# Kernel tuning notes

Measured on AMD Instinct MI355X. Metric: run time of the kernel, lower is better.

Reference implementation:

```python
import jax, jax.numpy as jnp
from jax import lax
import numpy as np

B, S, V, H, C = 128, 512, 128, 1024, 10
E = H // 4  # embed_dim = hidden_dim / 4 per the module


def setup_inputs() -> dict:
    key = jax.random.key(0)
    ks = jax.random.split(key, 16)

    def kaiming(k, shape):
        fan_in = shape[0]
        return jax.random.normal(k, shape, dtype=jnp.float32) * np.sqrt(2.0 / fan_in)

    return {
        "x": jax.random.randint(ks[0], (B, 1, S), 0, V),
        "embedding": jax.random.normal(ks[1], (V, E), dtype=jnp.float32),
        "W_gx": kaiming(ks[2], (E, H)), "W_gh": kaiming(ks[3], (H, H)), "b_g": jnp.zeros((H,), jnp.float32),
        "W_ix": kaiming(ks[4], (E, H)), "W_ih": kaiming(ks[5], (H, H)), "b_i": jnp.zeros((H,), jnp.float32),
        "W_fx": kaiming(ks[6], (E, H)), "W_fh": kaiming(ks[7], (H, H)), "b_f": jnp.zeros((H,), jnp.float32),
        "W_ox": kaiming(ks[8], (E, H)), "W_oh": kaiming(ks[9], (H, H)), "b_o": jnp.zeros((H,), jnp.float32),
        "W_ph": kaiming(ks[10], (H, C)), "b_p": jnp.zeros((C,), jnp.float32),
    }


def reference(x, embedding, W_gx, W_gh, b_g, W_ix, W_ih, b_i,
              W_fx, W_fh, b_f, W_ox, W_oh, b_o, W_ph, b_p):
    batch = x.shape[0]
    hid = W_gh.shape[0]
    # embed whole sequence at once: [B, S, E]
    xe = embedding[x[:, 0, :]]
    # fuse the 4 input-side GEMMs into one: [B, S, 4H] (precomputable, parallel over time)
    Wx = jnp.concatenate([W_gx, W_ix, W_fx, W_ox], axis=1)  # [E, 4H]
    Wh = jnp.concatenate([W_gh, W_ih, W_fh, W_oh], axis=1)  # [H, 4H]
    b = jnp.concatenate([b_g, b_i, b_f, b_o])               # [4H]
    xproj = jnp.einsum('bse,ef->sbf', xe, Wx) + b           # [S, B, 4H] (time-major for scan)

    def step(carry, xp_t):
        h, c = carry
        z = xp_t + h @ Wh  # [B, 4H]
        g = jnp.tanh(z[:, :hid])
        i = jax.nn.sigmoid(z[:, hid:2 * hid])
        f = jax.nn.sigmoid(z[:, 2 * hid:3 * hid])
        o = jax.nn.sigmoid(z[:, 3 * hid:])
        c = g * i + c * f
        h = jnp.tanh(c) * o
        return (h, c), None

    h0 = jnp.zeros((batch, hid), xproj.dtype)
    c0 = jnp.zeros((batch, hid), xproj.dtype)
    (h, _), _ = lax.scan(step, (h0, c0), xproj)

    p = h @ W_ph + b_p
    return jax.nn.log_softmax(p, axis=1)
```

## Files before the change

kernel.cpp:

```cpp
#include <hip/hip_runtime.h>

#define H_ 1024
#define B_ 128
#define S_ 512
#define V_ 128
#define E_ 256

#define ZSH_OFF 0
#define TSH_OFF 67584
#define HSH_OFF 135168
#define XSH_OFF 136192
#define SMEM_TOTAL 136256

#define HXBUF 131072

typedef __bf16 bf16x8 __attribute__((ext_vector_type(8)));
typedef float f32x4 __attribute__((ext_vector_type(4)));
typedef unsigned long long ull;

__device__ __forceinline__ uint4 cload16(const unsigned short* p) {
  uint4 r;
  asm volatile("global_load_dwordx4 %0, %1, off sc0 sc1"
               : "=v"(r) : "v"(p) : "memory");
  return r;
}
__device__ __forceinline__ void cstore8(unsigned short* p, ull v) {
  __hip_atomic_store((ull*)p, v, __ATOMIC_RELAXED, __HIP_MEMORY_SCOPE_AGENT);
}

__device__ __forceinline__ unsigned short f2bf(float f) {
  unsigned u = __float_as_uint(f);
  u += 0x7fffu + ((u >> 16) & 1u);
  return (unsigned short)(u >> 16);
}
__device__ __forceinline__ float sigf(float x) { return 1.0f / (1.0f + __expf(-x)); }
__device__ __forceinline__ float tanhfast(float x) { return 1.0f - 2.0f / (1.0f + __expf(2.0f * x)); }

__global__ void __launch_bounds__(256)
prep_kernel(const float* __restrict__ emb,
            const float* __restrict__ Wgx, const float* __restrict__ Wix,
            const float* __restrict__ Wfx, const float* __restrict__ Wox,
            const float* __restrict__ bg, const float* __restrict__ bi,
            const float* __restrict__ bf_, const float* __restrict__ bo,
            const float* __restrict__ Wgh, const float* __restrict__ Wih,
            const float* __restrict__ Wfh, const float* __restrict__ Woh,
            const int* __restrict__ x,
            float* __restrict__ tokproj, unsigned short* __restrict__ WhT,
            int* __restrict__ xT) {
  __shared__ float esh[E_];
  const int bid = blockIdx.x;
  if (bid < 2048) {
    const int v = bid >> 4;
    const int c = (bid & 15) * 256 + threadIdx.x;
    const int gate = c >> 10;
    const int j = c & 1023;
    const float* W = (gate == 0) ? Wgx : (gate == 1) ? Wix : (gate == 2) ? Wfx : Wox;
    const float* bias = (gate == 0) ? bg : (gate == 1) ? bi : (gate == 2) ? bf_ : bo;
    esh[threadIdx.x] = emb[v * E_ + threadIdx.x];
    __syncthreads();
    float acc = bias[j];
#pragma unroll 4
    for (int e = 0; e < E_; ++e) acc += esh[e] * W[e * H_ + j];
    tokproj[v * 4096 + c] = acc;
  } else if (bid < 6144) {
    const int c = bid - 2048;
    const int gate = c >> 10;
    const int j = c & 1023;
    const float* W = (gate == 0) ? Wgh : (gate == 1) ? Wih : (gate == 2) ? Wfh : Woh;
    for (int k = threadIdx.x; k < H_; k += 256)
      WhT[c * H_ + k] = f2bf(W[k * H_ + j]);
  } else {
    const int id = (bid - 6144) * 256 + threadIdx.x;
    const int s = id >> 7, b = id & 127;
    xT[s * 128 + b] = x[b * S_ + s];
  }
}

__global__ void __launch_bounds__(512, 1)
lstm_scan(const int* __restrict__ xT, const float* __restrict__ tokproj,
          const unsigned short* __restrict__ WhT,
          unsigned short* __restrict__ hX, float* __restrict__ hfin,
          unsigned* __restrict__ pub) {
  extern __shared__ char smem[];
  float* Zsh = (float*)(smem + ZSH_OFF);
  float* tsh = (float*)(smem + TSH_OFF);
  unsigned short* hsh = (unsigned short*)(smem + HSH_OFF);
  int* xsh = (int*)(smem + XSH_OFF);

  const int bid = blockIdx.x;
  const int rg = bid >> 5;
  const int cg = bid & 31;
  const int tid = threadIdx.x;
  const int w = tid >> 6;
  const int lane = tid & 63;
  const int l15 = lane & 15;
  const int lq = lane >> 4;

  for (int it = tid; it < 16384; it += 512) {
    const int v = it >> 7, j = it & 127;
    const int gate = j >> 5, hu = j & 31;
    tsh[(v * 33 + hu) * 4 + gate] = tokproj[v * 4096 + gate * 1024 + cg * 32 + hu];
  }
  uint4 breg[32];
#pragma unroll
  for (int kc = 0; kc < 4; ++kc) {
#pragma unroll
    for (int t = 0; t < 8; ++t) {
      const int j = t * 16 + l15;
      const int c = ((j >> 5) << 10) + cg * 32 + (j & 31);
      breg[kc * 8 + t] =
          *(const uint4*)(WhT + c * 1024 + (w * 4 + kc) * 32 + lq * 8);
    }
  }

  const int row_own = tid >> 5;
  const int hu = tid & 31;
  const int brow = rg * 16 + row_own;
  const int colg = cg * 32 + hu;

  const unsigned* myflag = pub + (rg * 32 + w * 4 + (lane & 3)) * 32;
  const unsigned short* abase[4];
#pragma unroll
  for (int kc = 0; kc < 4; ++kc)
    abase[kc] = hX + (rg * 32 + w * 4 + kc) * 512 + lane * 8;

  float creg = 0.f;
  if (tid < 128) cstore8(hX + bid * 512 + tid * 4, 0ull);
  asm volatile("s_waitcnt vmcnt(0)" ::: "memory");
  __syncthreads();
  if (tid == 0)
    __hip_atomic_store(pub + bid * 32, 1u, __ATOMIC_RELAXED, __HIP_MEMORY_SCOPE_AGENT);

  for (int s = 0; s < S_; ++s) {
    int xv = 0;
    if (tid < 16) xv = xT[s * 128 + rg * 16 + tid];

    const unsigned tgt = (unsigned)(s + 1);
    while (__hip_atomic_load(myflag, __ATOMIC_RELAXED, __HIP_MEMORY_SCOPE_AGENT) < tgt)
      __builtin_amdgcn_s_sleep(1);

    const int soff = (s & 1) * HXBUF;
    uint4 a[4];
#pragma unroll
    for (int kc = 0; kc < 4; ++kc) a[kc] = cload16(abase[kc] + soff);
    asm volatile("s_waitcnt vmcnt(0)" ::: "memory");
    __builtin_amdgcn_sched_barrier(0);
#pragma unroll
    for (int kc = 0; kc < 4; ++kc) {
      asm volatile("" : "+v"(a[kc].x), "+v"(a[kc].y), "+v"(a[kc].z), "+v"(a[kc].w));
    }

    if (tid < 16) xsh[tid] = xv;

    f32x4 acc[8];
#pragma unroll
    for (int t = 0; t < 8; ++t) acc[t] = (f32x4){0.f, 0.f, 0.f, 0.f};
#pragma unroll
    for (int kc = 0; kc < 4; ++kc) {
      const bf16x8 av = __builtin_bit_cast(bf16x8, a[kc]);
#pragma unroll
      for (int t = 0; t < 8; ++t)
        acc[t] = __builtin_amdgcn_mfma_f32_16x16x32_bf16(
            av, __builtin_bit_cast(bf16x8, breg[kc * 8 + t]), acc[t], 0, 0, 0);
    }
#pragma unroll
    for (int r_ = 0; r_ < 4; ++r_) {
      const int row = w * 16 + lq * 4 + r_;
      f32x4 lo = {acc[0][r_], acc[2][r_], acc[4][r_], acc[6][r_]};
      f32x4 hi = {acc[1][r_], acc[3][r_], acc[5][r_], acc[7][r_]};
      *(f32x4*)(Zsh + (row * 33 + l15) * 4) = lo;
      *(f32x4*)(Zsh + (row * 33 + l15 + 16) * 4) = hi;
    }
    __syncthreads();

    {
      const int xb = xsh[row_own];
      f32x4 z4 = *(const f32x4*)(tsh + (xb * 33 + hu) * 4);
#pragma unroll
      for (int w8 = 0; w8 < 8; ++w8)
        z4 += *(const f32x4*)(Zsh + ((w8 * 16 + row_own) * 33 + hu) * 4);
      const float gv = tanhfast(z4[0]);
      const float iv = sigf(z4[1]);
      const float fv = sigf(z4[2]);
      const float ov = sigf(z4[3]);
      creg = gv * iv + creg * fv;
      const float hv = tanhfast(creg) * ov;
      hsh[row_own * 32 + hu] = f2bf(hv);
      if (s == S_ - 1) hfin[brow * H_ + colg] = hv;
    }
    __syncthreads();

    if (tid < 64) {
      const ull* hp = (const ull*)hsh;
      const int si = (tid & 15) * 8 + (tid >> 4) * 2;
      unsigned short* dst = hX + ((s + 1) & 1) * HXBUF + bid * 512 + tid * 8;
      cstore8(dst, hp[si]);
      cstore8(dst + 4, hp[si + 1]);
      asm volatile("s_waitcnt vmcnt(0)" ::: "memory");
      if (tid == 0)
        __hip_atomic_store(pub + bid * 32, (unsigned)(s + 2),
                           __ATOMIC_RELAXED, __HIP_MEMORY_SCOPE_AGENT);
    }
  }
}

__global__ void __launch_bounds__(256)
classify_kernel(const float* __restrict__ hfin, const float* __restrict__ Wph,
                const float* __restrict__ bp, float* __restrict__ out) {
  __shared__ float red[256 * 10];
  const int b = blockIdx.x, tid = threadIdx.x;
  float acc[10];
#pragma unroll
  for (int c = 0; c < 10; ++c) acc[c] = 0.f;
  for (int k = tid; k < H_; k += 256) {
    const float hv = hfin[b * H_ + k];
    const float* w = Wph + k * 10;
#pragma unroll
    for (int c = 0; c < 10; ++c) acc[c] += hv * w[c];
  }
#pragma unroll
  for (int c = 0; c < 10; ++c) red[tid * 10 + c] = acc[c];
  __syncthreads();
  for (int off = 128; off >= 1; off >>= 1) {
    if (tid < off) {
#pragma unroll
      for (int c = 0; c < 10; ++c) red[tid * 10 + c] += red[(tid + off) * 10 + c];
    }
    __syncthreads();
  }
  if (tid == 0) {
    float p[10];
    float m = -1e30f;
#pragma unroll
    for (int c = 0; c < 10; ++c) { p[c] = red[c] + bp[c]; m = fmaxf(m, p[c]); }
    float ssum = 0.f;
#pragma unroll
    for (int c = 0; c < 10; ++c) ssum += __expf(p[c] - m);
    const float lse = m + __logf(ssum);
#pragma unroll
    for (int c = 0; c < 10; ++c) out[b * 10 + c] = p[c] - lse;
  }
}

extern "C" void kernel_launch(void* const* d_in, const int* in_sizes, int n_in,
                              void* d_out, int out_size, void* d_ws, size_t ws_size,
                              hipStream_t stream) {
  (void)in_sizes; (void)n_in; (void)out_size; (void)ws_size;
  const int* x = (const int*)d_in[0];
  const float* emb = (const float*)d_in[1];
  const float* Wgx = (const float*)d_in[2];
  const float* Wgh = (const float*)d_in[3];
  const float* bg = (const float*)d_in[4];
  const float* Wix = (const float*)d_in[5];
  const float* Wih = (const float*)d_in[6];
  const float* bi = (const float*)d_in[7];
  const float* Wfx = (const float*)d_in[8];
  const float* Wfh = (const float*)d_in[9];
  const float* bf_ = (const float*)d_in[10];
  const float* Wox = (const float*)d_in[11];
  const float* Woh = (const float*)d_in[12];
  const float* bo = (const float*)d_in[13];
  const float* Wph = (const float*)d_in[14];
  const float* bp = (const float*)d_in[15];
  float* out = (float*)d_out;

  char* ws = (char*)d_ws;
  float* tokproj = (float*)ws;
  unsigned short* WhT = (unsigned short*)(ws + 2097152);
  unsigned short* hX = (unsigned short*)(ws + 10485760);
  float* hfin = (float*)(ws + 11010048);
  int* xT = (int*)(ws + 11538432);
  unsigned* pub = (unsigned*)(ws + 11800576);

  (void)hipMemsetAsync(pub, 0, 32768, stream);
  (void)hipFuncSetAttribute(reinterpret_cast<const void*>(lstm_scan),
                            hipFuncAttributeMaxDynamicSharedMemorySize, SMEM_TOTAL);

  prep_kernel<<<dim3(6400), dim3(256), 0, stream>>>(
      emb, Wgx, Wix, Wfx, Wox, bg, bi, bf_, bo,
      Wgh, Wih, Wfh, Woh, x, tokproj, WhT, xT);
  lstm_scan<<<dim3(256), dim3(512), SMEM_TOTAL, stream>>>(
      xT, tokproj, WhT, hX, hfin, pub);
  classify_kernel<<<dim3(128), dim3(256), 0, stream>>>(hfin, Wph, bp, out);
}
```

Baseline: 1.709 ms.

## Replace flag-based inter-block sync with NaN-sentinel triple-buffered hidden state

Drops the per-block publish flags and signals readiness through sentinel values in the hidden-state buffers. It uses a triple buffer: each step resets the buffer two steps ahead to 0xFFFF patterns, and consumers spin-reload their h tiles until no sentinel remains. This removes the flag store/load round trip and the wait for the data stores before publishing, which shortens the serial per-step critical path. In exchange, spinning now re-reads full data tiles. Correctness depends on bf16 h never encoding as 0xFFFF and on ordering between the reset and the data stores. A guard counter also breaks out after a bounded number of spins, which could silently consume stale data.

```diff
diff --git a/kernel.cpp b/kernel.cpp
--- a/kernel.cpp
+++ b/kernel.cpp
@@ -17,6 +17,9 @@
 typedef __bf16 bf16x8 __attribute__((ext_vector_type(8)));
 typedef float f32x4 __attribute__((ext_vector_type(4)));
 typedef unsigned long long ull;
+
+#define NANP 0xFFFFFFFFu
+#define NAN8 0xFFFFFFFFFFFFFFFFull
 
 __device__ __forceinline__ uint4 cload16(const unsigned short* p) {
   uint4 r;
@@ -79,8 +82,7 @@
 __global__ void __launch_bounds__(512, 1)
 lstm_scan(const int* __restrict__ xT, const float* __restrict__ tokproj,
           const unsigned short* __restrict__ WhT,
-          unsigned short* __restrict__ hX, float* __restrict__ hfin,
-          unsigned* __restrict__ pub) {
+          unsigned short* __restrict__ hX, float* __restrict__ hfin) {
   extern __shared__ char smem[];
   float* Zsh = (float*)(smem + ZSH_OFF);
   float* tsh = (float*)(smem + TSH_OFF);
@@ -118,32 +120,46 @@
   const int brow = rg * 16 + row_own;
   const int colg = cg * 32 + hu;
 
-  const unsigned* myflag = pub + (rg * 32 + w * 4 + (lane & 3)) * 32;
   const unsigned short* abase[4];
 #pragma unroll
   for (int kc = 0; kc < 4; ++kc)
     abase[kc] = hX + (rg * 32 + w * 4 + kc) * 512 + lane * 8;
 
   float creg = 0.f;
-  if (tid < 128) cstore8(hX + bid * 512 + tid * 4, 0ull);
-  asm volatile("s_waitcnt vmcnt(0)" ::: "memory");
-  __syncthreads();
-  if (tid == 0)
-    __hip_atomic_store(pub + bid * 32, 1u, __ATOMIC_RELAXED, __HIP_MEMORY_SCOPE_AGENT);
+  if (tid < 64) {
+    unsigned short* dst = hX + bid * 512 + tid * 8;
+    cstore8(dst, 0ull);
+    cstore8(dst + 4, 0ull);
+  }
+
+  int bcur = 0;
+  int bnxt = 1;
+  int brst = 2;
 
   for (int s = 0; s < S_; ++s) {
     int xv = 0;
     if (tid < 16) xv = xT[s * 128 + rg * 16 + tid];
 
-    const unsigned tgt = (unsigned)(s + 1);
-    while (__hip_atomic_load(myflag, __ATOMIC_RELAXED, __HIP_MEMORY_SCOPE_AGENT) < tgt)
-      __builtin_amdgcn_s_sleep(1);
-
-    const int soff = (s & 1) * HXBUF;
+    const int soff = bcur * HXBUF;
     uint4 a[4];
-#pragma unroll
-    for (int kc = 0; kc < 4; ++kc) a[kc] = cload16(abase[kc] + soff);
-    asm volatile("s_waitcnt vmcnt(0)" ::: "memory");
+    {
+      int need0 = 1, need1 = 1, need2 = 1, need3 = 1;
+      int guard = 0;
+      for (;;) {
+        if (need0) a[0] = cload16(abase[0] + soff);
+        if (need1) a[1] = cload16(abase[1] + soff);
+        if (need2) a[2] = cload16(abase[2] + soff);
+        if (need3) a[3] = cload16(abase[3] + soff);
+        asm volatile("s_waitcnt vmcnt(0)" ::: "memory");
+        if (need0) need0 = !__all((int)((a[0].x != NANP) & (a[0].z != NANP)));
+        if (need1) need1 = !__all((int)((a[1].x != NANP) & (a[1].z != NANP)));
+        if (need2) need2 = !__all((int)((a[2].x != NANP) & (a[2].z != NANP)));
+        if (need3) need3 = !__all((int)((a[3].x != NANP) & (a[3].z != NANP)));
+        if (!(need0 | need1 | need2 | need3)) break;
+        if (++guard > (1 << 14)) break;
+        __builtin_amdgcn_s_sleep(1);
+      }
+    }
     __builtin_amdgcn_sched_barrier(0);
 #pragma unroll
     for (int kc = 0; kc < 4; ++kc) {
@@ -191,16 +207,17 @@
     __syncthreads();
 
     if (tid < 64) {
+      unsigned short* rdst = hX + brst * HXBUF + bid * 512 + tid * 8;
+      cstore8(rdst, NAN8);
+      cstore8(rdst + 4, NAN8);
+      asm volatile("s_waitcnt vmcnt(0)" ::: "memory");
       const ull* hp = (const ull*)hsh;
       const int si = (tid & 15) * 8 + (tid >> 4) * 2;
-      unsigned short* dst = hX + ((s + 1) & 1) * HXBUF + bid * 512 + tid * 8;
+      unsigned short* dst = hX + bnxt * HXBUF + bid * 512 + tid * 8;
       cstore8(dst, hp[si]);
       cstore8(dst + 4, hp[si + 1]);
-      asm volatile("s_waitcnt vmcnt(0)" ::: "memory");
-      if (tid == 0)
-        __hip_atomic_store(pub + bid * 32, (unsigned)(s + 2),
-                           __ATOMIC_RELAXED, __HIP_MEMORY_SCOPE_AGENT);
-    }
+    }
+    const int t_ = bcur; bcur = bnxt; bnxt = brst; brst = t_;
   }
 }
 
@@ -268,11 +285,10 @@
   float* tokproj = (float*)ws;
   unsigned short* WhT = (unsigned short*)(ws + 2097152);
   unsigned short* hX = (unsigned short*)(ws + 10485760);
-  float* hfin = (float*)(ws + 11010048);
-  int* xT = (int*)(ws + 11538432);
-  unsigned* pub = (unsigned*)(ws + 11800576);
-
-  (void)hipMemsetAsync(pub, 0, 32768, stream);
+  float* hfin = (float*)(ws + 11272192);
+  int* xT = (int*)(ws + 11796480);
+
+  (void)hipMemsetAsync(hX, 0xFF, 786432, stream);
   (void)hipFuncSetAttribute(reinterpret_cast<const void*>(lstm_scan),
                             hipFuncAttributeMaxDynamicSharedMemorySize, SMEM_TOTAL);
 
@@ -280,6 +296,6 @@
       emb, Wgx, Wix, Wfx, Wox, bg, bi, bf_, bo,
       Wgh, Wih, Wfh, Woh, x, tokproj, WhT, xT);
   lstm_scan<<<dim3(256), dim3(512), SMEM_TOTAL, stream>>>(
-      xT, tokproj, WhT, hX, hfin, pub);
+      xT, tokproj, WhT, hX, hfin);
   classify_kernel<<<dim3(128), dim3(256), 0, stream>>>(hfin, Wph, bp, out);
 }
```

New measurement: 1.928 ms. 12.8% more time.
